# Performance work log

Hardware: AMD Instinct MI355X
Metric: run time of the kernel (lower is better)

The kernel has to match this reference:

```python
import jax, jax.numpy as jnp
import numpy as np

B, S, DIM = 2, 2048, 2048
N_HEADS, N_KV_HEADS = 16, 4
HEAD_DIM = DIM // N_HEADS  # 128
N_REP = N_HEADS // N_KV_HEADS  # 4
ROPE_THETA = 10000.0


def setup_inputs() -> dict:
    key = jax.random.key(0)
    ks = jax.random.split(key, 6)
    x = jax.random.normal(ks[0], (B, S, DIM), dtype=jnp.float32)
    # torch nn.Linear weights are [out_features, in_features]
    sc = 0.02
    wq = jax.random.normal(ks[1], (N_HEADS * HEAD_DIM, DIM), dtype=jnp.float32) * sc
    wk = jax.random.normal(ks[2], (N_KV_HEADS * HEAD_DIM, DIM), dtype=jnp.float32) * sc
    wv = jax.random.normal(ks[3], (N_KV_HEADS * HEAD_DIM, DIM), dtype=jnp.float32) * sc
    wo = jax.random.normal(ks[4], (DIM, N_HEADS * HEAD_DIM), dtype=jnp.float32) * sc
    # precomputed rotary table (freqs_cis in llama): [S, head_dim//2]
    inv_freq = 1.0 / (ROPE_THETA ** (jnp.arange(0, HEAD_DIM, 2, dtype=jnp.float32) / HEAD_DIM))
    t = jnp.arange(S, dtype=jnp.float32)
    freqs = jnp.outer(t, inv_freq)  # [S, head_dim//2]
    freqs_cos = jnp.cos(freqs)
    freqs_sin = jnp.sin(freqs)
    # additive causal mask as passed to SDPA (float, 0 on allowed, -inf-like elsewhere)
    causal = jnp.tril(jnp.ones((S, S), dtype=bool))
    mask = jnp.where(causal, 0.0, -1e9).astype(jnp.float32)
    return {"x": x, "wq": wq, "wk": wk, "wv": wv, "wo": wo,
            "freqs_cos": freqs_cos, "freqs_sin": freqs_sin, "mask": mask}


def _apply_rope(t, cos, sin):
    # t: [B, S, H, D]; cos/sin: [S, D//2] -> complex multiply on adjacent pairs
    tr = t.reshape(*t.shape[:-1], -1, 2)  # [B,S,H,D/2,2]
    tre, tim = tr[..., 0], tr[..., 1]
    c = cos[None, :, None, :]
    s = sin[None, :, None, :]
    out_re = tre * c - tim * s
    out_im = tre * s + tim * c
    return jnp.stack([out_re, out_im], axis=-1).reshape(t.shape)


def reference(x, wq, wk, wv, wo, freqs_cos, freqs_sin, mask):
    Bx, Sx, _ = x.shape
    xq = (x @ wq.T).reshape(Bx, Sx, N_HEADS, HEAD_DIM)
    xk = (x @ wk.T).reshape(Bx, Sx, N_KV_HEADS, HEAD_DIM)
    xv = (x @ wv.T).reshape(Bx, Sx, N_KV_HEADS, HEAD_DIM)
    xq = _apply_rope(xq, freqs_cos, freqs_sin)
    xk = _apply_rope(xk, freqs_cos, freqs_sin)
    # repeat_kv for GQA: [B,S,KV,D] -> [B,S,KV*n_rep,D]
    keys = jnp.repeat(xk, N_REP, axis=2)
    values = jnp.repeat(xv, N_REP, axis=2)
    q = xq.transpose(0, 2, 1, 3)      # [B,H,S,D]
    k = keys.transpose(0, 2, 1, 3)
    v = values.transpose(0, 2, 1, 3)
    scale = 1.0 / jnp.sqrt(jnp.float32(HEAD_DIM))
    scores = jnp.einsum('bhqd,bhkd->bhqk', q, k) * scale + mask[None, None]
    attn = jax.nn.softmax(scores, axis=-1)
    out = jnp.einsum('bhqk,bhkd->bhqd', attn, v)
    out = out.transpose(0, 2, 1, 3).reshape(Bx, Sx, -1)
    return out @ wo.T
```

## Files before the change

kernel.cpp:

```cpp
#include <hip/hip_runtime.h>
#include <hip/hip_bf16.h>

#define B_   2
#define S_   2048
#define DIM_ 2048
#define NH   16
#define NKV  4
#define HD   128
#define QKVN 3072

typedef __attribute__((ext_vector_type(8)))  short  sv8;
typedef __attribute__((ext_vector_type(8)))  ushort usv8;
typedef __attribute__((ext_vector_type(4)))  float  fv4;
typedef __attribute__((ext_vector_type(16))) float  fv16;

__device__ __forceinline__ float fast_exp2(float x) {
  return __builtin_amdgcn_exp2f(x);
}

__device__ __forceinline__ ushort f2bf(float f) {
  __hip_bfloat16 h = __float2bfloat16(f);
  union { __hip_bfloat16 h; ushort u; } c; c.h = h; return c.u;
}
__device__ __forceinline__ float bf2f(ushort u) {
  union { unsigned int i; float f; } c; c.i = ((unsigned)u) << 16; return c.f;
}

__device__ __forceinline__ unsigned int cvtpk(float lo, float hi) {
  unsigned int r;
  asm("v_cvt_pk_bf16_f32 %0, %1, %2" : "=v"(r) : "v"(lo), "v"(hi));
  return r;
}
__device__ __forceinline__ unsigned int xhalf(unsigned int x) {
  return (unsigned int)__shfl_xor((int)x, 32, 64);
}

__device__ __forceinline__ float tmax16(const fv16& v) {
  float a = fmaxf(fmaxf(v[0], v[1]),  fmaxf(v[2], v[3]));
  float b = fmaxf(fmaxf(v[4], v[5]),  fmaxf(v[6], v[7]));
  float c = fmaxf(fmaxf(v[8], v[9]),  fmaxf(v[10], v[11]));
  float d = fmaxf(fmaxf(v[12], v[13]), fmaxf(v[14], v[15]));
  return fmaxf(fmaxf(a, b), fmaxf(c, d));
}
__device__ __forceinline__ float tsum16(const fv16& v) {
  float a = (v[0] + v[1]) + (v[2] + v[3]);
  float b = (v[4] + v[5]) + (v[6] + v[7]);
  float c = (v[8] + v[9]) + (v[10] + v[11]);
  float d = (v[12] + v[13]) + (v[14] + v[15]);
  return (a + b) + (c + d);
}

__device__ __forceinline__ void async16(const void* g, void* l) {
  __builtin_amdgcn_global_load_lds(
      (const __attribute__((address_space(1))) unsigned int*)g,
      (__attribute__((address_space(3))) unsigned int*)l, 16, 0, 0);
}

__global__ void cvt_kernel(const float* __restrict__ in, ushort* __restrict__ out, int n) {
  int i = (blockIdx.x * 256 + threadIdx.x) * 4;
  if (i >= n) return;
  fv4 v = *(const fv4*)(in + i);
  ushort4 o;
  o.x = f2bf(v[0]); o.y = f2bf(v[1]); o.z = f2bf(v[2]); o.w = f2bf(v[3]);
  *(ushort4*)(out + i) = o;
}

__global__ void rope_kernel(const ushort* __restrict__ raw, const float* __restrict__ fc,
                            const float* __restrict__ fs, ushort* __restrict__ out,
                            int heads, int rowstride, float scale) {
  int t = blockIdx.x * 256 + threadIdx.x;
  int grp = t & 15;
  int h   = (t >> 4) % heads;
  int s   = ((t >> 4) / heads) % S_;
  int b   = t / (16 * heads * S_);
  const ushort* src = raw + (size_t)(b * S_ + s) * rowstride + h * HD + grp * 8;
  sv8 v = *(const sv8*)src;
  fv4 c  = *(const fv4*)(fc + s * 64 + grp * 4);
  fv4 sn = *(const fv4*)(fs + s * 64 + grp * 4);
  sv8 o;
#pragma unroll
  for (int p = 0; p < 4; ++p) {
    float re = bf2f((ushort)v[2 * p]);
    float im = bf2f((ushort)v[2 * p + 1]);
    float orr = (re * c[p] - im * sn[p]) * scale;
    float oi  = (re * sn[p] + im * c[p]) * scale;
    o[2 * p]     = (short)f2bf(orr);
    o[2 * p + 1] = (short)f2bf(oi);
  }
  ushort* dst = out + ((size_t)(b * heads + h) * S_ + s) * HD + grp * 8;
  *(sv8*)dst = o;
}

__global__ __launch_bounds__(256) void vtrans_kernel(const ushort* __restrict__ vraw,
                                                     ushort* __restrict__ vt, int rowstride) {
  __shared__ ushort tile[128][136];
  int blk = blockIdx.x;
  int st  = blk & 15;
  int kvb = blk >> 4;
  int kv  = kvb & 3;
  int b   = kvb >> 2;
  int s0  = st << 7;
#pragma unroll
  for (int it = 0; it < 8; ++it) {
    int t = it * 256 + threadIdx.x;
    int srow = t >> 4;
    int d8 = (t & 15) * 8;
    usv8 v = *(const usv8*)(vraw + (size_t)(b * S_ + s0 + srow) * rowstride + kv * HD + d8);
#pragma unroll
    for (int j = 0; j < 8; ++j) tile[d8 + j][srow] = v[j];
  }
  __syncthreads();
#pragma unroll
  for (int it = 0; it < 8; ++it) {
    int t = it * 256 + threadIdx.x;
    int d = t >> 4;
    int s8 = (t & 15) * 8;
    usv8 o;
#pragma unroll
    for (int j = 0; j < 8; ++j) o[j] = tile[d][s8 + j];
    *(usv8*)(vt + ((size_t)(b * NKV + kv) * HD + d) * S_ + s0 + s8) = o;
  }
}

template <typename OutT>
__global__ __launch_bounds__(256) void gemm_bt(const ushort* __restrict__ A,
                                               const ushort* __restrict__ Bm,
                                               OutT* __restrict__ C,
                                               int M, int N, int K) {
  __shared__ ushort As[128 * 64];
  __shared__ ushort Bs[128 * 64];
  int nb = N >> 7;
  int bx = blockIdx.x % nb;
  int by = blockIdx.x / nb;
  int m0 = by << 7, n0 = bx << 7;
  int lane = threadIdx.x & 63, w = threadIdx.x >> 6;
  int l15 = lane & 15, lg = lane >> 4;
  int wm = (w >> 1) * 64, wn = (w & 1) * 64;

  const ushort* aSrc[4]; const ushort* bSrc[4];
  ushort* aDst[4]; ushort* bDst[4];
#pragma unroll
  for (int it = 0; it < 4; ++it) {
    int lin = it * 4096 + w * 1024 + lane * 16;
    int row = lin >> 7;
    int cb  = (lin & 127) ^ ((row & 7) << 4);
    aSrc[it] = A  + (size_t)(m0 + row) * K + (cb >> 1);
    bSrc[it] = Bm + (size_t)(n0 + row) * K + (cb >> 1);
    aDst[it] = As + ((it * 4096 + w * 1024) >> 1);
    bDst[it] = Bs + ((it * 4096 + w * 1024) >> 1);
  }

  fv4 acc[4][4] = {};

  for (int kt = 0; kt < K; kt += 64) {
#pragma unroll
    for (int it = 0; it < 4; ++it) async16(aSrc[it] + kt, aDst[it]);
#pragma unroll
    for (int it = 0; it < 4; ++it) async16(bSrc[it] + kt, bDst[it]);
    __syncthreads();
#pragma unroll
    for (int kk = 0; kk < 2; ++kk) {
      sv8 af[4], bfr[4];
#pragma unroll
      for (int i = 0; i < 4; ++i) {
        int row = wm + i * 16 + l15;
        int byt = row * 128 + ((kk * 64 + (lg << 4)) ^ ((row & 7) << 4));
        af[i] = *(const sv8*)((const char*)As + byt);
      }
#pragma unroll
      for (int j = 0; j < 4; ++j) {
        int row = wn + j * 16 + l15;
        int byt = row * 128 + ((kk * 64 + (lg << 4)) ^ ((row & 7) << 4));
        bfr[j] = *(const sv8*)((const char*)Bs + byt);
      }
#pragma unroll
      for (int i = 0; i < 4; ++i)
#pragma unroll
        for (int j = 0; j < 4; ++j)
          acc[i][j] = __builtin_amdgcn_mfma_f32_16x16x32_bf16(af[i], bfr[j], acc[i][j], 0, 0, 0);
    }
    __syncthreads();
  }

#pragma unroll
  for (int i = 0; i < 4; ++i)
#pragma unroll
    for (int j = 0; j < 4; ++j)
#pragma unroll
      for (int r = 0; r < 4; ++r) {
        int row = m0 + wm + i * 16 + (lg << 2) + r;
        int col = n0 + wn + j * 16 + l15;
        if constexpr (sizeof(OutT) == 2) C[(size_t)row * N + col] = (OutT)f2bf(acc[i][j][r]);
        else                             C[(size_t)row * N + col] = (OutT)acc[i][j][r];
      }
}

__global__ __launch_bounds__(512, 2) void attn_kernel(const ushort* __restrict__ Q,
                                                      const ushort* __restrict__ Kr,
                                                      const ushort* __restrict__ Vt,
                                                      ushort* __restrict__ O) {
  __shared__ __align__(16) ushort SMEM[65536];

  int blk = blockIdx.x;
  int bh  = blk & 31;
  int pr  = blk >> 5;
  int h   = bh & 15;
  int b   = bh >> 4;
  int kv  = h >> 2;
  int lane = threadIdx.x & 63, w = threadIdx.x >> 6;
  int wg = w & 3, Hf = w >> 2;
  int l31 = lane & 31, hh = lane >> 5;

  const ushort* Qbase = Q  + (size_t)(b * NH  + h ) * S_ * HD;
  const ushort* Kbase = Kr + (size_t)(b * NKV + kv) * S_ * HD;
  const ushort* Vbase = Vt + (size_t)(b * NKV + kv) * HD * S_;

  const ushort* kSrc[4]; ushort* kDst[2][4];
  const ushort* vSrc[4]; ushort* vDst[2][4];
#pragma unroll
  for (int it = 0; it < 4; ++it) {
    int lin = it * 4096 + wg * 1024 + lane * 16;
    { int row = lin >> 8; int cb = (lin & 255) ^ ((row & 7) << 4);
      kSrc[it] = Kbase + (size_t)row * HD + (cb >> 1); }
    { int row = lin >> 7; int cb = (lin & 127) ^ ((row & 7) << 4);
      vSrc[it] = Vbase + (size_t)row * S_ + (cb >> 1); }
#pragma unroll
    for (int buf = 0; buf < 2; ++buf) {
      kDst[buf][it] = SMEM + Hf * 16384 + buf * 8192 + ((it * 4096 + wg * 1024) >> 1);
      vDst[buf][it] = SMEM + 32768 + Hf * 16384 + buf * 8192 + ((it * 4096 + wg * 1024) >> 1);
    }
  }

  float* cML = (float*)SMEM;
  float* cO  = (float*)SMEM + 512;

  for (int pass = 0; pass < 2; ++pass) {
    int qt = pass ? (15 - pr) : pr;
    int q0 = qt << 7;
    int qrow_w = q0 + wg * 32;
    int myq    = qrow_w + l31;
    int nj     = qt + 1;
    int ktbase = Hf * nj;

    sv8 qf[8];
#pragma unroll
    for (int kk = 0; kk < 8; ++kk)
      qf[kk] = *(const sv8*)(Qbase + (size_t)myq * HD + kk * 16 + hh * 8);

    fv16 oacc[4] = {};
    float mrun = -1e30f, lrun = 0.f;

    {
      size_t k0 = (size_t)ktbase << 6;
#pragma unroll
      for (int it = 0; it < 4; ++it) async16(kSrc[it] + k0 * HD, kDst[0][it]);
#pragma unroll
      for (int it = 0; it < 4; ++it) async16(vSrc[it] + k0,      vDst[0][it]);
    }

    for (int j = 0; j < nj; ++j) {
      int cur = j & 1, nxt = cur ^ 1;
      __syncthreads();
      if (j + 1 < nj) {
        size_t k0n = (size_t)(ktbase + j + 1) << 6;
#pragma unroll
        for (int it = 0; it < 4; ++it) async16(kSrc[it] + k0n * HD, kDst[nxt][it]);
#pragma unroll
        for (int it = 0; it < 4; ++it) async16(vSrc[it] + k0n,      vDst[nxt][it]);
      }
      const char* KsC = (const char*)(SMEM + Hf * 16384 + cur * 8192);
      const char* VsC = (const char*)(SMEM + 32768 + Hf * 16384 + cur * 8192);
      int k0 = (ktbase + j) << 6;

      fv16 sacc[2] = {};
      __builtin_amdgcn_s_setprio(1);
#pragma unroll
      for (int kk = 0; kk < 8; ++kk) {
        int cb = kk * 32 + hh * 16;
        int r0 = l31, r1 = 32 + l31;
        sv8 kf0 = *(const sv8*)(KsC + r0 * 256 + (cb ^ ((r0 & 7) << 4)));
        sv8 kf1 = *(const sv8*)(KsC + r1 * 256 + (cb ^ ((r1 & 7) << 4)));
        sacc[0] = __builtin_amdgcn_mfma_f32_32x32x16_bf16(kf0, qf[kk], sacc[0], 0, 0, 0);
        sacc[1] = __builtin_amdgcn_mfma_f32_32x32x16_bf16(kf1, qf[kk], sacc[1], 0, 0, 0);
      }
      __builtin_amdgcn_s_setprio(0);

      if (k0 + 63 > qrow_w) {
        int thr = myq - k0 - 4 * hh;
#pragma unroll
        for (int t = 0; t < 2; ++t)
#pragma unroll
          for (int r = 0; r < 16; ++r) {
            int kp = t * 32 + (r & 3) + 8 * (r >> 2);
            if (kp > thr) sacc[t][r] = -1e38f;
          }
      }

      float tmax = fmaxf(tmax16(sacc[0]), tmax16(sacc[1]));
      tmax = fmaxf(tmax, __shfl_xor(tmax, 32, 64));

      if (__any(tmax > mrun + 8.0f)) {
        float mnew = fmaxf(mrun, tmax);
        float esc  = fast_exp2(mrun - mnew);
        lrun *= esc;
        float er[16];
#pragma unroll
        for (int r = 0; r < 16; ++r) er[r] = __shfl(esc, (r & 3) + 8 * (r >> 2) + 4 * hh, 64);
#pragma unroll
        for (int d0 = 0; d0 < 4; ++d0)
#pragma unroll
          for (int r = 0; r < 16; ++r) oacc[d0][r] *= er[r];
        mrun = mnew;
      }

#pragma unroll
      for (int t = 0; t < 2; ++t)
#pragma unroll
        for (int r = 0; r < 16; ++r) sacc[t][r] = fast_exp2(sacc[t][r] - mrun);
      float psum = tsum16(sacc[0]) + tsum16(sacc[1]);
      psum += __shfl_xor(psum, 32, 64);
      lrun += psum;

      union Frag { unsigned int u[4]; sv8 v; } pa[4];
#pragma unroll
      for (int t = 0; t < 2; ++t)
#pragma unroll
        for (int half = 0; half < 2; ++half) {
          int cb = half * 8;
          unsigned int a0 = cvtpk(sacc[t][cb + 0], sacc[t][cb + 1]);
          unsigned int a1 = cvtpk(sacc[t][cb + 2], sacc[t][cb + 3]);
          unsigned int b0 = cvtpk(sacc[t][cb + 4], sacc[t][cb + 5]);
          unsigned int b1 = cvtpk(sacc[t][cb + 6], sacc[t][cb + 7]);
          unsigned int a0p = xhalf(a0), a1p = xhalf(a1);
          unsigned int b0p = xhalf(b0), b1p = xhalf(b1);
          pa[2 * t + half].u[0] = hh ? b0p : a0;
          pa[2 * t + half].u[1] = hh ? b1p : a1;
          pa[2 * t + half].u[2] = hh ? b0  : a0p;
          pa[2 * t + half].u[3] = hh ? b1  : a1p;
        }

      __builtin_amdgcn_s_setprio(1);
#pragma unroll
      for (int ks = 0; ks < 4; ++ks) {
        int cb = ks * 32 + hh * 16;
#pragma unroll
        for (int d0 = 0; d0 < 4; ++d0) {
          int row = d0 * 32 + l31;
          sv8 vf = *(const sv8*)(VsC + row * 128 + (cb ^ ((row & 7) << 4)));
          oacc[d0] = __builtin_amdgcn_mfma_f32_32x32x16_bf16(pa[ks].v, vf, oacc[d0], 0, 0, 0);
        }
      }
      __builtin_amdgcn_s_setprio(0);
    }

    __syncthreads();
    if (Hf) {
      int base = wg * 64 + lane;
      cML[base * 2]     = mrun;
      cML[base * 2 + 1] = lrun;
      float* dst = cO + base * 65;
#pragma unroll
      for (int d0 = 0; d0 < 4; ++d0)
#pragma unroll
        for (int r = 0; r < 16; ++r) dst[d0 * 16 + r] = oacc[d0][r];
    }
    __syncthreads();
    if (!Hf) {
      int base = wg * 64 + lane;
      float m2 = cML[base * 2], l2 = cML[base * 2 + 1];
      const float* src = cO + base * 65;
      float m  = fmaxf(mrun, m2);
      float e1 = fast_exp2(mrun - m), e2 = fast_exp2(m2 - m);
      float l  = lrun * e1 + l2 * e2;
      float inv = 1.0f / l;
      float f1 = e1 * inv, f2 = e2 * inv;
      float f1b[16], f2b[16];
#pragma unroll
      for (int r = 0; r < 16; ++r) {
        int ro = (r & 3) + 8 * (r >> 2) + 4 * hh;
        f1b[r] = __shfl(f1, ro, 64);
        f2b[r] = __shfl(f2, ro, 64);
      }
#pragma unroll
      for (int r = 0; r < 16; ++r) {
        int q = qrow_w + (r & 3) + 8 * (r >> 2) + 4 * hh;
#pragma unroll
        for (int d0 = 0; d0 < 4; ++d0) {
          int d = d0 * 32 + l31;
          float val = oacc[d0][r] * f1b[r] + src[d0 * 16 + r] * f2b[r];
          O[(size_t)(b * S_ + q) * DIM_ + h * HD + d] = f2bf(val);
        }
      }
    }
    __syncthreads();
  }
}

extern "C" void kernel_launch(void* const* d_in, const int* in_sizes, int n_in,
                              void* d_out, int out_size, void* d_ws, size_t ws_size,
                              hipStream_t stream) {
  const float* x  = (const float*)d_in[0];
  const float* wq = (const float*)d_in[1];
  const float* wk = (const float*)d_in[2];
  const float* wv = (const float*)d_in[3];
  const float* wo = (const float*)d_in[4];
  const float* fc = (const float*)d_in[5];
  const float* fs = (const float*)d_in[6];
  float* out = (float*)d_out;

  char* ws = (char*)d_ws;
  size_t off = 0;
  auto alloc = [&](size_t bytes) -> ushort* {
    ushort* p = (ushort*)(ws + off);
    off += (bytes + 255) & ~(size_t)255;
    return p;
  };
  ushort* xb    = alloc((size_t)B_ * S_ * DIM_ * 2);
  ushort* wqkvb = alloc((size_t)QKVN * DIM_ * 2);
  ushort* wob   = alloc((size_t)DIM_ * DIM_ * 2);
  ushort* qkvr  = alloc((size_t)B_ * S_ * QKVN * 2);
  ushort* qr    = alloc((size_t)B_ * S_ * DIM_ * 2);
  ushort* kr    = alloc((size_t)B_ * S_ * NKV * HD * 2);
  ushort* vtb   = alloc((size_t)B_ * S_ * NKV * HD * 2);
  ushort* obf   = alloc((size_t)B_ * S_ * DIM_ * 2);
  (void)ws_size; (void)n_in; (void)in_sizes; (void)out_size;

  cvt_kernel<<<(B_ * S_ * DIM_) / 1024, 256, 0, stream>>>(x,  xb, B_ * S_ * DIM_);
  cvt_kernel<<<(DIM_ * DIM_) / 1024,     256, 0, stream>>>(wq, wqkvb,                 DIM_ * DIM_);
  cvt_kernel<<<(NKV * HD * DIM_) / 1024, 256, 0, stream>>>(wk, wqkvb + 2048 * DIM_,   NKV * HD * DIM_);
  cvt_kernel<<<(NKV * HD * DIM_) / 1024, 256, 0, stream>>>(wv, wqkvb + 2560 * DIM_,   NKV * HD * DIM_);
  cvt_kernel<<<(DIM_ * DIM_) / 1024,     256, 0, stream>>>(wo, wob, DIM_ * DIM_);

  gemm_bt<ushort><<<(B_ * S_ / 128) * (QKVN / 128), 256, 0, stream>>>(xb, wqkvb, qkvr,
                                                                     B_ * S_, QKVN, DIM_);

  const float qscale = 0.08838834764831845f * 1.4426950408889634f;
  rope_kernel<<<(B_ * S_ * NH  * 16) / 256, 256, 0, stream>>>(qkvr,        fc, fs, qr, NH,  QKVN, qscale);
  rope_kernel<<<(B_ * S_ * NKV * 16) / 256, 256, 0, stream>>>(qkvr + 2048, fc, fs, kr, NKV, QKVN, 1.0f);
  vtrans_kernel<<<B_ * NKV * (S_ / 128), 256, 0, stream>>>(qkvr + 2560, vtb, QKVN);

  attn_kernel<<<B_ * NH * 8, 512, 0, stream>>>(qr, kr, vtb, obf);

  gemm_bt<float><<<(B_ * S_ / 128) * (DIM_ / 128), 256, 0, stream>>>(obf, wob, out, B_ * S_, DIM_, DIM_);
}
```

Measured before the change: 201.5 us.

## Replace 128x128 GEMM with 256x256 double-buffered, barrier-interleaved MFMA pipeline

Replaces the simple 128x128-tile GEMM, which loads and then computes with a barrier between the two, with a 256x256-tile, 512-thread kernel. The new kernel double-buffers LDS tiles, prefetches two K-steps ahead, and splits each step into four MFMA phases with interleaved LDS reads and async global loads. The goal is more data reuse per tile and global-load latency hidden behind compute. In exchange it uses more registers, 128 KB of LDS, many barriers, and far fewer blocks: 192 for QKV and 128 for the output projection, which may underfill 256 CUs.

```diff
diff --git a/kernel.cpp b/kernel.cpp
--- a/kernel.cpp
+++ b/kernel.cpp
@@ -123,75 +123,154 @@
 }
 
 template <typename OutT>
-__global__ __launch_bounds__(256) void gemm_bt(const ushort* __restrict__ A,
-                                               const ushort* __restrict__ Bm,
-                                               OutT* __restrict__ C,
-                                               int M, int N, int K) {
-  __shared__ ushort As[128 * 64];
-  __shared__ ushort Bs[128 * 64];
-  int nb = N >> 7;
-  int bx = blockIdx.x % nb;
-  int by = blockIdx.x / nb;
-  int m0 = by << 7, n0 = bx << 7;
-  int lane = threadIdx.x & 63, w = threadIdx.x >> 6;
+__global__ __launch_bounds__(512, 2) void gemm256(const ushort* __restrict__ A,
+                                                  const ushort* __restrict__ Bm,
+                                                  OutT* __restrict__ C,
+                                                  int M, int N, int K) {
+  __shared__ __align__(16) ushort SM[65536];
+  int nb = N >> 8;
+  int bx = blockIdx.x % nb, by = blockIdx.x / nb;
+  int m0 = by << 8, n0 = bx << 8;
+  int tid = threadIdx.x;
+  int lane = tid & 63, w = tid >> 6;
   int l15 = lane & 15, lg = lane >> 4;
-  int wm = (w >> 1) * 64, wn = (w & 1) * 64;
-
-  const ushort* aSrc[4]; const ushort* bSrc[4];
-  ushort* aDst[4]; ushort* bDst[4];
-#pragma unroll
-  for (int it = 0; it < 4; ++it) {
-    int lin = it * 4096 + w * 1024 + lane * 16;
-    int row = lin >> 7;
-    int cb  = (lin & 127) ^ ((row & 7) << 4);
-    aSrc[it] = A  + (size_t)(m0 + row) * K + (cb >> 1);
-    bSrc[it] = Bm + (size_t)(n0 + row) * K + (cb >> 1);
-    aDst[it] = As + ((it * 4096 + w * 1024) >> 1);
-    bDst[it] = Bs + ((it * 4096 + w * 1024) >> 1);
-  }
-
-  fv4 acc[4][4] = {};
-
-  for (int kt = 0; kt < K; kt += 64) {
-#pragma unroll
-    for (int it = 0; it < 4; ++it) async16(aSrc[it] + kt, aDst[it]);
-#pragma unroll
-    for (int it = 0; it < 4; ++it) async16(bSrc[it] + kt, bDst[it]);
-    __syncthreads();
-#pragma unroll
-    for (int kk = 0; kk < 2; ++kk) {
-      sv8 af[4], bfr[4];
-#pragma unroll
-      for (int i = 0; i < 4; ++i) {
-        int row = wm + i * 16 + l15;
-        int byt = row * 128 + ((kk * 64 + (lg << 4)) ^ ((row & 7) << 4));
-        af[i] = *(const sv8*)((const char*)As + byt);
-      }
-#pragma unroll
-      for (int j = 0; j < 4; ++j) {
-        int row = wn + j * 16 + l15;
-        int byt = row * 128 + ((kk * 64 + (lg << 4)) ^ ((row & 7) << 4));
-        bfr[j] = *(const sv8*)((const char*)Bs + byt);
-      }
-#pragma unroll
-      for (int i = 0; i < 4; ++i)
-#pragma unroll
-        for (int j = 0; j < 4; ++j)
-          acc[i][j] = __builtin_amdgcn_mfma_f32_16x16x32_bf16(af[i], bfr[j], acc[i][j], 0, 0, 0);
-    }
-    __syncthreads();
-  }
-
-#pragma unroll
-  for (int i = 0; i < 4; ++i)
+  int wm = (w >> 2) * 128;
+  int wn = (w & 3) * 64;
+  int pA = (w >> 2);
+  int pB = 2 + ((w & 3) >> 1);
+  int brow0 = (w & 1) * 64;
+
+  int srow = tid >> 3;
+  int cb   = ((tid & 7) * 16) ^ ((srow & 7) << 4);
+  const ushort* sA0 = A  + (size_t)(m0 + srow) * K + (cb >> 1);
+  const ushort* sB0 = Bm + (size_t)(n0 + srow) * K + (cb >> 1);
+  const ushort* srcs[4] = { sA0, sA0 + (size_t)128 * K, sB0, sB0 + (size_t)128 * K };
+  size_t rstep = (size_t)64 * K;
+
+  int nkt = K >> 6;
+
+  auto STG = [&](int part, int t, int db) {
+    ushort* d0 = SM + db * 32768 + part * 8192 + (w << 9);
+    const ushort* s0 = srcs[part] + t * 64;
+    async16(s0, d0);
+    async16(s0 + rstep, d0 + 4096);
+  };
+
+  fv4 acc[8][4] = {};
+  sv8 a[4][2], b[2][2], b2[2][2];
+
+#pragma unroll
+  for (int p = 0; p < 4; ++p) STG(p, 0, 0);
+  {
+    int t1 = 1 < nkt ? 1 : 0;
+#pragma unroll
+    for (int p = 0; p < 4; ++p) STG(p, t1, 1);
+  }
+  asm volatile("s_waitcnt vmcnt(8)");
+  __builtin_amdgcn_s_barrier();
+
+  for (int t = 0; t < nkt; ++t) {
+    int db = t & 1;
+    int t2 = t + 2 < nkt ? t + 2 : nkt - 1;
+    const char* Ab = (const char*)SM + db * 65536 + pA * 16384;
+    const char* Bb = (const char*)SM + db * 65536 + pB * 16384;
+
+#pragma unroll
+    for (int m = 0; m < 4; ++m)
+#pragma unroll
+      for (int kk = 0; kk < 2; ++kk) {
+        int row = m * 16 + l15;
+        a[m][kk] = *(const sv8*)(Ab + row * 128 + ((kk * 64 + lg * 16) ^ ((row & 7) << 4)));
+      }
+#pragma unroll
+    for (int j = 0; j < 2; ++j)
+#pragma unroll
+      for (int kk = 0; kk < 2; ++kk) {
+        int row = brow0 + j * 16 + l15;
+        b[j][kk] = *(const sv8*)(Bb + row * 128 + ((kk * 64 + lg * 16) ^ ((row & 7) << 4)));
+      }
+    __builtin_amdgcn_s_barrier();
+    asm volatile("s_waitcnt lgkmcnt(0)");
+    __builtin_amdgcn_s_setprio(1);
+#pragma unroll
+    for (int m = 0; m < 4; ++m)
+#pragma unroll
+      for (int j = 0; j < 2; ++j)
+#pragma unroll
+        for (int kk = 0; kk < 2; ++kk)
+          acc[m][j] = __builtin_amdgcn_mfma_f32_16x16x32_bf16(a[m][kk], b[j][kk], acc[m][j], 0, 0, 0);
+    __builtin_amdgcn_s_setprio(0);
+    __builtin_amdgcn_s_barrier();
+
+#pragma unroll
+    for (int j = 0; j < 2; ++j)
+#pragma unroll
+      for (int kk = 0; kk < 2; ++kk) {
+        int row = brow0 + (j + 2) * 16 + l15;
+        b2[j][kk] = *(const sv8*)(Bb + row * 128 + ((kk * 64 + lg * 16) ^ ((row & 7) << 4)));
+      }
+    __builtin_amdgcn_s_barrier();
+    asm volatile("s_waitcnt lgkmcnt(0)");
+    __builtin_amdgcn_s_setprio(1);
+#pragma unroll
+    for (int m = 0; m < 4; ++m)
+#pragma unroll
+      for (int j = 0; j < 2; ++j)
+#pragma unroll
+        for (int kk = 0; kk < 2; ++kk)
+          acc[m][j + 2] = __builtin_amdgcn_mfma_f32_16x16x32_bf16(a[m][kk], b2[j][kk], acc[m][j + 2], 0, 0, 0);
+    __builtin_amdgcn_s_setprio(0);
+    __builtin_amdgcn_s_barrier();
+
+#pragma unroll
+    for (int m = 0; m < 4; ++m)
+#pragma unroll
+      for (int kk = 0; kk < 2; ++kk) {
+        int row = 64 + m * 16 + l15;
+        a[m][kk] = *(const sv8*)(Ab + row * 128 + ((kk * 64 + lg * 16) ^ ((row & 7) << 4)));
+      }
+    STG(2, t2, db);
+    STG(3, t2, db);
+    __builtin_amdgcn_s_barrier();
+    asm volatile("s_waitcnt lgkmcnt(0)");
+    __builtin_amdgcn_s_setprio(1);
+#pragma unroll
+    for (int m = 0; m < 4; ++m)
+#pragma unroll
+      for (int j = 0; j < 2; ++j)
+#pragma unroll
+        for (int kk = 0; kk < 2; ++kk)
+          acc[m + 4][j + 2] = __builtin_amdgcn_mfma_f32_16x16x32_bf16(a[m][kk], b2[j][kk], acc[m + 4][j + 2], 0, 0, 0);
+    __builtin_amdgcn_s_setprio(0);
+    __builtin_amdgcn_s_barrier();
+
+    STG(0, t2, db);
+    STG(1, t2, db);
+    asm volatile("s_waitcnt vmcnt(8)");
+    __builtin_amdgcn_s_barrier();
+    __builtin_amdgcn_s_setprio(1);
+#pragma unroll
+    for (int m = 0; m < 4; ++m)
+#pragma unroll
+      for (int j = 0; j < 2; ++j)
+#pragma unroll
+        for (int kk = 0; kk < 2; ++kk)
+          acc[m + 4][j] = __builtin_amdgcn_mfma_f32_16x16x32_bf16(a[m][kk], b[j][kk], acc[m + 4][j], 0, 0, 0);
+    __builtin_amdgcn_s_setprio(0);
+    __builtin_amdgcn_s_barrier();
+  }
+
+  asm volatile("s_waitcnt vmcnt(0)");
+#pragma unroll
+  for (int m = 0; m < 8; ++m)
 #pragma unroll
     for (int j = 0; j < 4; ++j)
 #pragma unroll
       for (int r = 0; r < 4; ++r) {
-        int row = m0 + wm + i * 16 + (lg << 2) + r;
+        int row = m0 + wm + m * 16 + lg * 4 + r;
         int col = n0 + wn + j * 16 + l15;
-        if constexpr (sizeof(OutT) == 2) C[(size_t)row * N + col] = (OutT)f2bf(acc[i][j][r]);
-        else                             C[(size_t)row * N + col] = (OutT)acc[i][j][r];
+        if constexpr (sizeof(OutT) == 2) C[(size_t)row * N + col] = (OutT)f2bf(acc[m][j][r]);
+        else                             C[(size_t)row * N + col] = (OutT)acc[m][j][r];
       }
 }
 
@@ -220,10 +299,10 @@
 #pragma unroll
   for (int it = 0; it < 4; ++it) {
     int lin = it * 4096 + wg * 1024 + lane * 16;
-    { int row = lin >> 8; int cb = (lin & 255) ^ ((row & 7) << 4);
-      kSrc[it] = Kbase + (size_t)row * HD + (cb >> 1); }
-    { int row = lin >> 7; int cb = (lin & 127) ^ ((row & 7) << 4);
-      vSrc[it] = Vbase + (size_t)row * S_ + (cb >> 1); }
+    { int row = lin >> 8; int cbv = (lin & 255) ^ ((row & 7) << 4);
+      kSrc[it] = Kbase + (size_t)row * HD + (cbv >> 1); }
+    { int row = lin >> 7; int cbv = (lin & 127) ^ ((row & 7) << 4);
+      vSrc[it] = Vbase + (size_t)row * S_ + (cbv >> 1); }
 #pragma unroll
     for (int buf = 0; buf < 2; ++buf) {
       kDst[buf][it] = SMEM + Hf * 16384 + buf * 8192 + ((it * 4096 + wg * 1024) >> 1);
@@ -276,10 +355,10 @@
       __builtin_amdgcn_s_setprio(1);
 #pragma unroll
       for (int kk = 0; kk < 8; ++kk) {
-        int cb = kk * 32 + hh * 16;
+        int cbq = kk * 32 + hh * 16;
         int r0 = l31, r1 = 32 + l31;
-        sv8 kf0 = *(const sv8*)(KsC + r0 * 256 + (cb ^ ((r0 & 7) << 4)));
-        sv8 kf1 = *(const sv8*)(KsC + r1 * 256 + (cb ^ ((r1 & 7) << 4)));
+        sv8 kf0 = *(const sv8*)(KsC + r0 * 256 + (cbq ^ ((r0 & 7) << 4)));
+        sv8 kf1 = *(const sv8*)(KsC + r1 * 256 + (cbq ^ ((r1 & 7) << 4)));
         sacc[0] = __builtin_amdgcn_mfma_f32_32x32x16_bf16(kf0, qf[kk], sacc[0], 0, 0, 0);
         sacc[1] = __builtin_amdgcn_mfma_f32_32x32x16_bf16(kf1, qf[kk], sacc[1], 0, 0, 0);
       }
@@ -326,11 +405,11 @@
       for (int t = 0; t < 2; ++t)
 #pragma unroll
         for (int half = 0; half < 2; ++half) {
-          int cb = half * 8;
-          unsigned int a0 = cvtpk(sacc[t][cb + 0], sacc[t][cb + 1]);
-          unsigned int a1 = cvtpk(sacc[t][cb + 2], sacc[t][cb + 3]);
-          unsigned int b0 = cvtpk(sacc[t][cb + 4], sacc[t][cb + 5]);
-          unsigned int b1 = cvtpk(sacc[t][cb + 6], sacc[t][cb + 7]);
+          int cbq = half * 8;
+          unsigned int a0 = cvtpk(sacc[t][cbq + 0], sacc[t][cbq + 1]);
+          unsigned int a1 = cvtpk(sacc[t][cbq + 2], sacc[t][cbq + 3]);
+          unsigned int b0 = cvtpk(sacc[t][cbq + 4], sacc[t][cbq + 5]);
+          unsigned int b1 = cvtpk(sacc[t][cbq + 6], sacc[t][cbq + 7]);
           unsigned int a0p = xhalf(a0), a1p = xhalf(a1);
           unsigned int b0p = xhalf(b0), b1p = xhalf(b1);
           pa[2 * t + half].u[0] = hh ? b0p : a0;
@@ -342,11 +421,11 @@
       __builtin_amdgcn_s_setprio(1);
 #pragma unroll
       for (int ks = 0; ks < 4; ++ks) {
-        int cb = ks * 32 + hh * 16;
+        int cbq = ks * 32 + hh * 16;
 #pragma unroll
         for (int d0 = 0; d0 < 4; ++d0) {
           int row = d0 * 32 + l31;
-          sv8 vf = *(const sv8*)(VsC + row * 128 + (cb ^ ((row & 7) << 4)));
+          sv8 vf = *(const sv8*)(VsC + row * 128 + (cbq ^ ((row & 7) << 4)));
           oacc[d0] = __builtin_amdgcn_mfma_f32_32x32x16_bf16(pa[ks].v, vf, oacc[d0], 0, 0, 0);
         }
       }
@@ -431,7 +510,7 @@
   cvt_kernel<<<(NKV * HD * DIM_) / 1024, 256, 0, stream>>>(wv, wqkvb + 2560 * DIM_,   NKV * HD * DIM_);
   cvt_kernel<<<(DIM_ * DIM_) / 1024,     256, 0, stream>>>(wo, wob, DIM_ * DIM_);
 
-  gemm_bt<ushort><<<(B_ * S_ / 128) * (QKVN / 128), 256, 0, stream>>>(xb, wqkvb, qkvr,
+  gemm256<ushort><<<(B_ * S_ / 256) * (QKVN / 256), 512, 0, stream>>>(xb, wqkvb, qkvr,
                                                                      B_ * S_, QKVN, DIM_);
 
   const float qscale = 0.08838834764831845f * 1.4426950408889634f;
@@ -441,5 +520,5 @@
 
   attn_kernel<<<B_ * NH * 8, 512, 0, stream>>>(qr, kr, vtb, obf);
 
-  gemm_bt<float><<<(B_ * S_ / 128) * (DIM_ / 128), 256, 0, stream>>>(obf, wob, out, B_ * S_, DIM_, DIM_);
-}
+  gemm256<float><<<(B_ * S_ / 256) * (DIM_ / 256), 512, 0, stream>>>(obf, wob, out, B_ * S_, DIM_, DIM_);
+}
```

Result: slower. 210.5 us (+4.5%).
